# Optimization experiments

Hardware: AMD Instinct MI355X
Metric: run time of the kernel (lower is better)

Reference implementation:

```python
import jax, jax.numpy as jnp
import numpy as np

H = 2048        # hidden_size
I = 1408        # moe_intermediate_size
E = 8           # n_routed_experts
TOP_K = 2       # num_experts_per_tok
N_SHARED = 2
IS = N_SHARED * I  # shared expert intermediate


def setup_inputs() -> dict:
    key = jax.random.key(0)
    ks = jax.random.split(key, 8)
    s_h = 1.0 / np.sqrt(H)
    s_i = 1.0 / np.sqrt(I)
    s_is = 1.0 / np.sqrt(IS)
    return {
        "hidden_states": jax.random.normal(ks[0], (1, 2048, H), jnp.float32),
        "gate_w": jax.random.normal(ks[1], (E, H), jnp.float32) * s_h,
        "w_gate": jax.random.normal(ks[2], (E, H, I), jnp.float32) * s_h,
        "w_up": jax.random.normal(ks[3], (E, H, I), jnp.float32) * s_h,
        "w_down": jax.random.normal(ks[4], (E, I, H), jnp.float32) * s_i,
        "sw_gate": jax.random.normal(ks[5], (H, IS), jnp.float32) * s_h,
        "sw_up": jax.random.normal(ks[6], (H, IS), jnp.float32) * s_h,
        "sw_down": jax.random.normal(ks[7], (IS, H), jnp.float32) * s_is,
    }


def reference(hidden_states, gate_w, w_gate, w_up, w_down, sw_gate, sw_up, sw_down):
    B, S, _ = hidden_states.shape
    x = hidden_states.reshape(-1, H)          # [N, H]
    N = x.shape[0]

    # --- gate: softmax over expert logits, then top-k (DeepSeek greedy gate) ---
    logits = x @ gate_w.T                      # [N, E]
    scores = jax.nn.softmax(logits, axis=-1)
    topk_w, topk_i = jax.lax.top_k(scores, TOP_K)   # [N, K]

    # --- routed experts: dense compute per expert, masked combine ---
    g = jnp.einsum('nh,ehi->eni', x, w_gate)   # [E, N, I]
    u = jnp.einsum('nh,ehi->eni', x, w_up)
    h = jax.nn.silu(g) * u
    eo = jnp.einsum('eni,eih->enh', h, w_down)  # [E, N, H]

    # combine weights: scatter top-k softmax scores into [N, E]
    combine = jnp.zeros((N, E), x.dtype).at[jnp.arange(N)[:, None], topk_i].add(topk_w)
    y = jnp.einsum('ne,enh->nh', combine, eo)  # weighted scatter-reduce combine

    # --- shared experts (always-on SwiGLU MLP) ---
    sh = jax.nn.silu(x @ sw_gate) * (x @ sw_up)
    y = y + sh @ sw_down

    return y.reshape(B, S, H)
```

## Files before the change

### kernel.cpp

```cpp
#include <hip/hip_runtime.h>
#include <hip/hip_bf16.h>

#define H    2048
#define NI   1408
#define NE   8
#define NTOK 2048
#define NIS  2816

typedef __bf16 bf16x8 __attribute__((ext_vector_type(8)));
typedef float  f32x4  __attribute__((ext_vector_type(4)));

#define ASYNC16(gp, lp) __builtin_amdgcn_global_load_lds( \
    (const __attribute__((address_space(1))) void*)(gp),  \
    (__attribute__((address_space(3))) void*)(lp), 16, 0, 0)

__global__ __launch_bounds__(256)
void cvt_kernel(const float* __restrict__ in, __bf16* __restrict__ out)
{
    size_t i = ((size_t)blockIdx.x * 256 + threadIdx.x) * 8;
    float4 v0 = *(const float4*)(in + i);
    float4 v1 = *(const float4*)(in + i + 4);
    union { __bf16 b[8]; uint4 u; } p;
    p.b[0] = (__bf16)v0.x; p.b[1] = (__bf16)v0.y;
    p.b[2] = (__bf16)v0.z; p.b[3] = (__bf16)v0.w;
    p.b[4] = (__bf16)v1.x; p.b[5] = (__bf16)v1.y;
    p.b[6] = (__bf16)v1.z; p.b[7] = (__bf16)v1.w;
    *(uint4*)(out + i) = p.u;
}

__global__ __launch_bounds__(256)
void cvt_t_kernel(const float* __restrict__ in, __bf16* __restrict__ out,
                  int K, int N)
{
    const size_t zoff = (size_t)blockIdx.z * K * N;
    in  += zoff;
    out += zoff;
    const int n0 = blockIdx.x * 64;
    const int k0 = blockIdx.y * 64;
    __shared__ __bf16 tile[64][72];
    const int t = threadIdx.x;
    const int tr  = t >> 4;
    const int tc4 = (t & 15) * 4;
#pragma unroll
    for (int i = 0; i < 4; ++i) {
        int k = i * 16 + tr;
        float4 v = *(const float4*)(in + (size_t)(k0 + k) * N + n0 + tc4);
        tile[k][tc4 + 0] = (__bf16)v.x;
        tile[k][tc4 + 1] = (__bf16)v.y;
        tile[k][tc4 + 2] = (__bf16)v.z;
        tile[k][tc4 + 3] = (__bf16)v.w;
    }
    __syncthreads();
    const int n = t >> 2, q = t & 3;
#pragma unroll
    for (int hh = 0; hh < 2; ++hh) {
        int qq = q + hh * 4;
        union { __bf16 b[8]; uint4 u; } pk;
#pragma unroll
        for (int j = 0; j < 8; ++j) pk.b[j] = tile[qq * 8 + j][n];
        *(uint4*)(out + (size_t)(n0 + n) * K + k0 + qq * 8) = pk.u;
    }
}

__global__ __launch_bounds__(256)
void gate_kernel(const float* __restrict__ x, const float* __restrict__ gw,
                 float* __restrict__ topw, int* __restrict__ pairs,
                 int* __restrict__ cnt)
{
    int tok  = blockIdx.x * 4 + (threadIdx.x >> 6);
    int lane = threadIdx.x & 63;
    float acc[NE];
#pragma unroll
    for (int e = 0; e < NE; ++e) acc[e] = 0.f;
    const float* xr = x + (size_t)tok * H;
    for (int h = lane; h < H; h += 64) {
        float xv = xr[h];
#pragma unroll
        for (int e = 0; e < NE; ++e) acc[e] += xv * gw[e * H + h];
    }
#pragma unroll
    for (int e = 0; e < NE; ++e) {
        float v = acc[e];
        for (int off = 32; off; off >>= 1) v += __shfl_xor(v, off);
        acc[e] = v;
    }
    if (lane == 0) {
        float mx = acc[0];
#pragma unroll
        for (int e = 1; e < NE; ++e) mx = fmaxf(mx, acc[e]);
        float p[NE]; float s = 0.f;
#pragma unroll
        for (int e = 0; e < NE; ++e) { p[e] = __expf(acc[e] - mx); s += p[e]; }
        float inv = 1.f / s;
        int e1 = 0;
#pragma unroll
        for (int e = 1; e < NE; ++e) if (acc[e] > acc[e1]) e1 = e;
        int e2 = -1;
#pragma unroll
        for (int e = 0; e < NE; ++e) {
            if (e == e1) continue;
            if (e2 < 0 || acc[e] > acc[e2]) e2 = e;
        }
        topw[tok * 2 + 0] = p[e1] * inv;
        topw[tok * 2 + 1] = p[e2] * inv;
        int pos1 = atomicAdd(&cnt[e1], 1);
        pairs[e1 * NTOK + pos1] = tok * 2 + 0;
        int pos2 = atomicAdd(&cnt[e2], 1);
        pairs[e2 * NTOK + pos2] = tok * 2 + 1;
    }
}

__global__ __launch_bounds__(256, 2)
void gu_kernel(const __bf16* __restrict__ xb,
               const __bf16* __restrict__ wgT, const __bf16* __restrict__ wuT,
               const __bf16* __restrict__ swgT, const __bf16* __restrict__ swuT,
               __bf16* __restrict__ h_sh, __bf16* __restrict__ h_rt,
               const int* __restrict__ pairs, const int* __restrict__ cnt)
{
    const int t = threadIdx.x, lane = t & 63;
    const int wid = t >> 6, wm = wid >> 1, wn = wid & 1;
    const int e = blockIdx.z;
    const bool routed = (e < NE);
    const int m0 = blockIdx.y * 128, n0 = blockIdx.x * 128;

    int count = NTOK;
    const __bf16 *Bg, *Bu;
    __bf16* outp;
    int ldO;
    if (routed) {
        if (n0 >= NI) return;
        count = cnt[e];
        if (m0 >= count) return;
        Bg = wgT + (size_t)e * NI * H;
        Bu = wuT + (size_t)e * NI * H;
        outp = h_rt; ldO = NI;
    } else {
        Bg = swgT; Bu = swuT; outp = h_sh; ldO = NIS;
    }

    __shared__ __align__(16) __bf16 At[128 * 32], Btg[128 * 32], Btu[128 * 32];
    __shared__ int tile_pid[128];
    if (t < 128) {
        int j = m0 + t;
        tile_pid[t] = routed ? ((j < count) ? pairs[e * NTOK + j] : -1) : j;
    }
    __syncthreads();

    const int r = t >> 2, c = t & 3;
    size_t ar0, ar1;
    if (routed) {
        int p0 = tile_pid[r];      if (p0 < 0) p0 = 0;
        int p1 = tile_pid[r + 64]; if (p1 < 0) p1 = 0;
        ar0 = (size_t)(p0 >> 1); ar1 = (size_t)(p1 >> 1);
    } else {
        ar0 = (size_t)(m0 + r); ar1 = (size_t)(m0 + r + 64);
    }
    const __bf16* a0 = xb + ar0 * H + c * 8;
    const __bf16* a1 = xb + ar1 * H + c * 8;
    const __bf16* g0 = Bg + (size_t)(n0 + r) * H + c * 8;
    const __bf16* g1 = Bg + (size_t)(n0 + r + 64) * H + c * 8;
    const __bf16* u0 = Bu + (size_t)(n0 + r) * H + c * 8;
    const __bf16* u1 = Bu + (size_t)(n0 + r + 64) * H + c * 8;
    __bf16* lA0 = At  + t * 8;  __bf16* lA1 = At  + (256 + t) * 8;
    __bf16* lG0 = Btg + t * 8;  __bf16* lG1 = Btg + (256 + t) * 8;
    __bf16* lU0 = Btu + t * 8;  __bf16* lU1 = Btu + (256 + t) * 8;

    f32x4 accg[4][4] = {};
    f32x4 accu[4][4] = {};

    for (int k0 = 0; k0 < H; k0 += 32) {
        __syncthreads();
        ASYNC16(a0 + k0, lA0); ASYNC16(a1 + k0, lA1);
        ASYNC16(g0 + k0, lG0); ASYNC16(g1 + k0, lG1);
        ASYNC16(u0 + k0, lU0); ASYNC16(u1 + k0, lU1);
        __syncthreads();
        bf16x8 a[4];
#pragma unroll
        for (int mi = 0; mi < 4; ++mi)
            a[mi] = *(const bf16x8*)(At + (wm * 64 + mi * 16 + (lane & 15)) * 32 + (lane >> 4) * 8);
#pragma unroll
        for (int ni = 0; ni < 4; ++ni) {
            bf16x8 bg = *(const bf16x8*)(Btg + (wn * 64 + ni * 16 + (lane & 15)) * 32 + (lane >> 4) * 8);
            bf16x8 bu = *(const bf16x8*)(Btu + (wn * 64 + ni * 16 + (lane & 15)) * 32 + (lane >> 4) * 8);
#pragma unroll
            for (int mi = 0; mi < 4; ++mi) {
                accg[mi][ni] = __builtin_amdgcn_mfma_f32_16x16x32_bf16(a[mi], bg, accg[mi][ni], 0, 0, 0);
                accu[mi][ni] = __builtin_amdgcn_mfma_f32_16x16x32_bf16(a[mi], bu, accu[mi][ni], 0, 0, 0);
            }
        }
    }

#pragma unroll
    for (int mi = 0; mi < 4; ++mi) {
#pragma unroll
        for (int rr = 0; rr < 4; ++rr) {
            int row = wm * 64 + mi * 16 + (lane >> 4) * 4 + rr;
            int pid = tile_pid[row];
            if (routed && pid < 0) continue;
            size_t orow = routed ? (size_t)pid : (size_t)(m0 + row);
#pragma unroll
            for (int ni = 0; ni < 4; ++ni) {
                int col = n0 + wn * 64 + ni * 16 + (lane & 15);
                float g = accg[mi][ni][rr];
                float u = accu[mi][ni][rr];
                float hv = g / (1.f + __expf(-g)) * u;
                outp[orow * (size_t)ldO + col] = (__bf16)hv;
            }
        }
    }
}

__global__ __launch_bounds__(256, 2)
void down_kernel(const __bf16* __restrict__ h_sh, const __bf16* __restrict__ h_rt,
                 const __bf16* __restrict__ swdT, const __bf16* __restrict__ wdT,
                 float* __restrict__ out,
                 const int* __restrict__ pairs, const int* __restrict__ cnt,
                 const float* __restrict__ topw)
{
    const int t = threadIdx.x, lane = t & 63;
    const int wid = t >> 6, wm = wid >> 1, wn = wid & 1;
    const int e = blockIdx.z;
    const bool routed = (e < NE);
    const int m0 = blockIdx.y * 128, n0 = blockIdx.x * 128;

    int count = NTOK, K, lda, koff = 0;
    const __bf16 *A, *B;
    if (routed) {
        count = cnt[e];
        if (m0 >= count) return;
        A = h_rt; lda = NI; K = NI;
        B = wdT + (size_t)e * H * NI;
    } else {
        A = h_sh; lda = NIS; K = NI;
        koff = (e == NE) ? 0 : NI;
        B = swdT;
    }

    __shared__ __align__(16) __bf16 At[128 * 32], Bt[128 * 32];
    __shared__ int tile_pid[128];
    if (t < 128) {
        int j = m0 + t;
        tile_pid[t] = routed ? ((j < count) ? pairs[e * NTOK + j] : -1) : j;
    }
    __syncthreads();

    const int r = t >> 2, c = t & 3;
    size_t ar0, ar1;
    if (routed) {
        int p0 = tile_pid[r];      if (p0 < 0) p0 = 0;
        int p1 = tile_pid[r + 64]; if (p1 < 0) p1 = 0;
        ar0 = (size_t)p0; ar1 = (size_t)p1;
    } else {
        ar0 = (size_t)(m0 + r); ar1 = (size_t)(m0 + r + 64);
    }
    const __bf16* a0 = A + ar0 * lda + koff + c * 8;
    const __bf16* a1 = A + ar1 * lda + koff + c * 8;
    const __bf16* b0 = B + (size_t)(n0 + r) * lda + koff + c * 8;
    const __bf16* b1 = B + (size_t)(n0 + r + 64) * lda + koff + c * 8;
    __bf16* lA0 = At + t * 8;  __bf16* lA1 = At + (256 + t) * 8;
    __bf16* lB0 = Bt + t * 8;  __bf16* lB1 = Bt + (256 + t) * 8;

    f32x4 acc[4][4] = {};

    for (int k0 = 0; k0 < K; k0 += 32) {
        __syncthreads();
        ASYNC16(a0 + k0, lA0); ASYNC16(a1 + k0, lA1);
        ASYNC16(b0 + k0, lB0); ASYNC16(b1 + k0, lB1);
        __syncthreads();
        bf16x8 a[4];
#pragma unroll
        for (int mi = 0; mi < 4; ++mi)
            a[mi] = *(const bf16x8*)(At + (wm * 64 + mi * 16 + (lane & 15)) * 32 + (lane >> 4) * 8);
#pragma unroll
        for (int ni = 0; ni < 4; ++ni) {
            bf16x8 b = *(const bf16x8*)(Bt + (wn * 64 + ni * 16 + (lane & 15)) * 32 + (lane >> 4) * 8);
#pragma unroll
            for (int mi = 0; mi < 4; ++mi)
                acc[mi][ni] = __builtin_amdgcn_mfma_f32_16x16x32_bf16(a[mi], b, acc[mi][ni], 0, 0, 0);
        }
    }

#pragma unroll
    for (int mi = 0; mi < 4; ++mi) {
#pragma unroll
        for (int rr = 0; rr < 4; ++rr) {
            int row = wm * 64 + mi * 16 + (lane >> 4) * 4 + rr;
            int pid = tile_pid[row];
            if (routed && pid < 0) continue;
            size_t tok; float w;
            if (routed) { tok = (size_t)(pid >> 1); w = topw[pid]; }
            else        { tok = (size_t)(m0 + row); w = 1.f; }
#pragma unroll
            for (int ni = 0; ni < 4; ++ni) {
                int col = n0 + wn * 64 + ni * 16 + (lane & 15);
                atomicAdd(out + tok * H + col, w * acc[mi][ni][rr]);
            }
        }
    }
}

extern "C" void kernel_launch(void* const* d_in, const int* in_sizes, int n_in,
                              void* d_out, int out_size, void* d_ws, size_t ws_size,
                              hipStream_t stream)
{
    const float* x       = (const float*)d_in[0];
    const float* gate_w  = (const float*)d_in[1];
    const float* w_gate  = (const float*)d_in[2];
    const float* w_up    = (const float*)d_in[3];
    const float* w_down  = (const float*)d_in[4];
    const float* sw_gate = (const float*)d_in[5];
    const float* sw_up   = (const float*)d_in[6];
    const float* sw_down = (const float*)d_in[7];

    char*   ws    = (char*)d_ws;
    float*  topw  = (float*)ws;
    int*    cnt   = (int*)(ws + 16384);
    int*    pairs = (int*)(ws + 16512);
    __bf16* xb    = (__bf16*)(ws + 131072);
    __bf16* h_sh  = (__bf16*)(ws + 8519680);
    __bf16* h_rt  = (__bf16*)(ws + 20054016);
    __bf16* swgT  = (__bf16*)(ws + 31588352);
    __bf16* swuT  = (__bf16*)(ws + 43122688);
    __bf16* swdT  = (__bf16*)(ws + 54657024);
    __bf16* wgT   = (__bf16*)(ws + 66191360);
    __bf16* wuT   = (__bf16*)(ws + 112328704);
    __bf16* wdT   = wgT;

    hipMemsetAsync(cnt, 0, NE * sizeof(int), stream);
    hipMemsetAsync(d_out, 0, (size_t)NTOK * H * sizeof(float), stream);

    cvt_kernel<<<NTOK * H / 2048, 256, 0, stream>>>(x, xb);
    cvt_t_kernel<<<dim3(NIS / 64, H / 64, 1), 256, 0, stream>>>(sw_gate, swgT, H, NIS);
    cvt_t_kernel<<<dim3(NIS / 64, H / 64, 1), 256, 0, stream>>>(sw_up,   swuT, H, NIS);
    cvt_t_kernel<<<dim3(H / 64, NIS / 64, 1), 256, 0, stream>>>(sw_down, swdT, NIS, H);
    cvt_t_kernel<<<dim3(NI / 64, H / 64, NE), 256, 0, stream>>>(w_gate,  wgT,  H, NI);
    cvt_t_kernel<<<dim3(NI / 64, H / 64, NE), 256, 0, stream>>>(w_up,    wuT,  H, NI);

    gate_kernel<<<NTOK / 4, 256, 0, stream>>>(x, gate_w, topw, pairs, cnt);

    gu_kernel<<<dim3(NIS / 128, NTOK / 128, NE + 1), 256, 0, stream>>>(
        xb, wgT, wuT, swgT, swuT, h_sh, h_rt, pairs, cnt);

    cvt_t_kernel<<<dim3(H / 64, NI / 64, NE), 256, 0, stream>>>(w_down, wdT, NI, H);

    down_kernel<<<dim3(H / 128, NTOK / 128, NE + 2), 256, 0, stream>>>(
        h_sh, h_rt, swdT, wdT, (float*)d_out, pairs, cnt, topw);
}
```

Measured before the change: 687.6 us.

## Rewrite gate/up GEMM with 256x256 tiles, interleaved weights and double-buffered LDS pipeline

The gate and up weights are interleaved in 128-row blocks during conversion, so one 256-wide B tile covers both gate and up columns. The gu kernel moves to 512 threads with 256x256 tiles, a double-buffered swizzled LDS pipeline using async global-to-LDS loads, explicit waitcnt and barriers, and raised priority around MFMA bursts. Up-projection accumulators are passed to the gate warps through LDS for the SiLU epilogue. This targets better data reuse and overlap of loads with MFMA, at the cost of 128KB of LDS per block, lower occupancy, and more padding waste for small routed expert counts.

Result: slower. 723.7 us (+5.2%).

```diff
diff --git a/kernel.cpp b/kernel.cpp
--- a/kernel.cpp
+++ b/kernel.cpp
@@ -13,6 +13,8 @@
 #define ASYNC16(gp, lp) __builtin_amdgcn_global_load_lds( \
     (const __attribute__((address_space(1))) void*)(gp),  \
     (__attribute__((address_space(3))) void*)(lp), 16, 0, 0)
+
+#define MFMA16 __builtin_amdgcn_mfma_f32_16x16x32_bf16
 
 __global__ __launch_bounds__(256)
 void cvt_kernel(const float* __restrict__ in, __bf16* __restrict__ out)
@@ -30,11 +32,10 @@
 
 __global__ __launch_bounds__(256)
 void cvt_t_kernel(const float* __restrict__ in, __bf16* __restrict__ out,
-                  int K, int N)
-{
-    const size_t zoff = (size_t)blockIdx.z * K * N;
-    in  += zoff;
-    out += zoff;
+                  int K, int N, int pmode)
+{
+    in  += (size_t)blockIdx.z * K * N;
+    out += (size_t)blockIdx.z * (pmode < 0 ? (size_t)K * N : 2 * (size_t)K * N);
     const int n0 = blockIdx.x * 64;
     const int k0 = blockIdx.y * 64;
     __shared__ __bf16 tile[64][72];
@@ -58,7 +59,10 @@
         union { __bf16 b[8]; uint4 u; } pk;
 #pragma unroll
         for (int j = 0; j < 8; ++j) pk.b[j] = tile[qq * 8 + j][n];
-        *(uint4*)(out + (size_t)(n0 + n) * K + k0 + qq * 8) = pk.u;
+        int gn = n0 + n;
+        size_t orow = (pmode < 0) ? (size_t)gn
+                    : ((size_t)((gn >> 7) * 2 + pmode) * 128 + (gn & 127));
+        *(uint4*)(out + orow * K + k0 + qq * 8) = pk.u;
     }
 }
 
@@ -110,104 +114,177 @@
     }
 }
 
-__global__ __launch_bounds__(256, 2)
+#define NT (H / 64)
+
+__global__ __launch_bounds__(512, 2)
 void gu_kernel(const __bf16* __restrict__ xb,
-               const __bf16* __restrict__ wgT, const __bf16* __restrict__ wuT,
-               const __bf16* __restrict__ swgT, const __bf16* __restrict__ swuT,
+               const __bf16* __restrict__ wguT, const __bf16* __restrict__ swguT,
                __bf16* __restrict__ h_sh, __bf16* __restrict__ h_rt,
                const int* __restrict__ pairs, const int* __restrict__ cnt)
 {
     const int t = threadIdx.x, lane = t & 63;
-    const int wid = t >> 6, wm = wid >> 1, wn = wid & 1;
+    const int wid = t >> 6;
+    const int wm = wid & 1;
+    const int wn = wid >> 1;
     const int e = blockIdx.z;
     const bool routed = (e < NE);
-    const int m0 = blockIdx.y * 128, n0 = blockIdx.x * 128;
+    const int sb = blockIdx.x;
+    const int m0 = blockIdx.y * 256;
 
     int count = NTOK;
-    const __bf16 *Bg, *Bu;
+    const __bf16* Bp;
     __bf16* outp;
     int ldO;
     if (routed) {
-        if (n0 >= NI) return;
+        if (sb >= NI / 128) return;
         count = cnt[e];
         if (m0 >= count) return;
-        Bg = wgT + (size_t)e * NI * H;
-        Bu = wuT + (size_t)e * NI * H;
+        Bp = wguT + (size_t)e * (2 * NI * H) + (size_t)sb * 256 * H;
         outp = h_rt; ldO = NI;
     } else {
-        Bg = swgT; Bu = swuT; outp = h_sh; ldO = NIS;
-    }
-
-    __shared__ __align__(16) __bf16 At[128 * 32], Btg[128 * 32], Btu[128 * 32];
-    __shared__ int tile_pid[128];
-    if (t < 128) {
+        Bp = swguT + (size_t)sb * 256 * H;
+        outp = h_sh; ldO = NIS;
+    }
+
+    __shared__ __align__(16) __bf16 sm[65536];
+    __shared__ int tile_pid[256];
+#define AH(buf, kk) (sm + ((buf) * 2 + (kk)) * 8192)
+#define BH(buf, kk) (sm + 32768 + ((buf) * 2 + (kk)) * 8192)
+
+    if (t < 256) {
         int j = m0 + t;
         tile_pid[t] = routed ? ((j < count) ? pairs[e * NTOK + j] : -1) : j;
     }
     __syncthreads();
 
-    const int r = t >> 2, c = t & 3;
+    const int sr = t >> 2;
+    const int cg = (t & 3) ^ ((t >> 3) & 3);
     size_t ar0, ar1;
     if (routed) {
-        int p0 = tile_pid[r];      if (p0 < 0) p0 = 0;
-        int p1 = tile_pid[r + 64]; if (p1 < 0) p1 = 0;
+        int p0 = tile_pid[sr];        if (p0 < 0) p0 = 0;
+        int p1 = tile_pid[128 + sr];  if (p1 < 0) p1 = 0;
         ar0 = (size_t)(p0 >> 1); ar1 = (size_t)(p1 >> 1);
     } else {
-        ar0 = (size_t)(m0 + r); ar1 = (size_t)(m0 + r + 64);
-    }
-    const __bf16* a0 = xb + ar0 * H + c * 8;
-    const __bf16* a1 = xb + ar1 * H + c * 8;
-    const __bf16* g0 = Bg + (size_t)(n0 + r) * H + c * 8;
-    const __bf16* g1 = Bg + (size_t)(n0 + r + 64) * H + c * 8;
-    const __bf16* u0 = Bu + (size_t)(n0 + r) * H + c * 8;
-    const __bf16* u1 = Bu + (size_t)(n0 + r + 64) * H + c * 8;
-    __bf16* lA0 = At  + t * 8;  __bf16* lA1 = At  + (256 + t) * 8;
-    __bf16* lG0 = Btg + t * 8;  __bf16* lG1 = Btg + (256 + t) * 8;
-    __bf16* lU0 = Btu + t * 8;  __bf16* lU1 = Btu + (256 + t) * 8;
-
-    f32x4 accg[4][4] = {};
-    f32x4 accu[4][4] = {};
-
-    for (int k0 = 0; k0 < H; k0 += 32) {
-        __syncthreads();
-        ASYNC16(a0 + k0, lA0); ASYNC16(a1 + k0, lA1);
-        ASYNC16(g0 + k0, lG0); ASYNC16(g1 + k0, lG1);
-        ASYNC16(u0 + k0, lU0); ASYNC16(u1 + k0, lU1);
-        __syncthreads();
-        bf16x8 a[4];
-#pragma unroll
-        for (int mi = 0; mi < 4; ++mi)
-            a[mi] = *(const bf16x8*)(At + (wm * 64 + mi * 16 + (lane & 15)) * 32 + (lane >> 4) * 8);
-#pragma unroll
-        for (int ni = 0; ni < 4; ++ni) {
-            bf16x8 bg = *(const bf16x8*)(Btg + (wn * 64 + ni * 16 + (lane & 15)) * 32 + (lane >> 4) * 8);
-            bf16x8 bu = *(const bf16x8*)(Btu + (wn * 64 + ni * 16 + (lane & 15)) * 32 + (lane >> 4) * 8);
-#pragma unroll
-            for (int mi = 0; mi < 4; ++mi) {
-                accg[mi][ni] = __builtin_amdgcn_mfma_f32_16x16x32_bf16(a[mi], bg, accg[mi][ni], 0, 0, 0);
-                accu[mi][ni] = __builtin_amdgcn_mfma_f32_16x16x32_bf16(a[mi], bu, accu[mi][ni], 0, 0, 0);
+        ar0 = (size_t)(m0 + sr); ar1 = (size_t)(m0 + 128 + sr);
+    }
+    const __bf16* gA0 = xb + ar0 * H + cg * 8;
+    const __bf16* gA1 = xb + ar1 * H + cg * 8;
+    const __bf16* gB0 = Bp + (size_t)sr * H + cg * 8;
+    const __bf16* gB1 = Bp + (size_t)(128 + sr) * H + cg * 8;
+
+#define STAGE_A(T, kk, buf) do {                              \
+        ASYNC16(gA0 + (T) * 64 + (kk) * 32, AH(buf, kk) + t * 8);        \
+        ASYNC16(gA1 + (T) * 64 + (kk) * 32, AH(buf, kk) + 4096 + t * 8); \
+    } while (0)
+#define STAGE_B(T, kk, buf) do {                              \
+        ASYNC16(gB0 + (T) * 64 + (kk) * 32, BH(buf, kk) + t * 8);        \
+        ASYNC16(gB1 + (T) * 64 + (kk) * 32, BH(buf, kk) + 4096 + t * 8); \
+    } while (0)
+
+    const int fr  = lane & 15;
+    const int cr8 = (((lane >> 4) ^ ((fr >> 1) & 3)) << 3);
+    const int aoff = (wm * 128 + fr) * 32 + cr8;
+    const int boff = (wn * 64  + fr) * 32 + cr8;
+
+    f32x4 acc[8][4] = {};
+    bf16x8 a[8], b[2];
+
+    STAGE_A(0, 0, 0); STAGE_B(0, 0, 0);
+    STAGE_A(0, 1, 0); STAGE_B(0, 1, 0);
+    STAGE_A(1, 0, 1); STAGE_B(1, 0, 1);
+    asm volatile("s_waitcnt vmcnt(4)" ::: "memory");
+    __builtin_amdgcn_s_barrier();
+
+#define PHASE_MFMA(NHB)                                       \
+    __builtin_amdgcn_s_barrier();                             \
+    asm volatile("s_waitcnt lgkmcnt(0)" ::: "memory");        \
+    __builtin_amdgcn_sched_barrier(0);                        \
+    __builtin_amdgcn_s_setprio(1);                            \
+    _Pragma("unroll")                                         \
+    for (int mi = 0; mi < 8; ++mi) {                          \
+        acc[mi][(NHB) + 0] = MFMA16(a[mi], b[0], acc[mi][(NHB) + 0], 0, 0, 0); \
+        acc[mi][(NHB) + 1] = MFMA16(a[mi], b[1], acc[mi][(NHB) + 1], 0, 0, 0); \
+    }                                                         \
+    __builtin_amdgcn_s_setprio(0);                            \
+    __builtin_amdgcn_s_barrier();
+
+#define TILE(TT, BUF) do {                                                   \
+                \
+    _Pragma("unroll")                                                        \
+    for (int mi = 0; mi < 8; ++mi)                                           \
+        a[mi] = *(const bf16x8*)(AH(BUF, 0) + aoff + mi * 512);              \
+    b[0] = *(const bf16x8*)(BH(BUF, 0) + boff);                              \
+    b[1] = *(const bf16x8*)(BH(BUF, 0) + boff + 512);                        \
+    if ((TT) + 1 < NT) { STAGE_A((TT) + 1, 1, (BUF) ^ 1);                    \
+                         STAGE_B((TT) + 1, 1, (BUF) ^ 1); }                  \
+    PHASE_MFMA(0)                                                            \
+                                                    \
+    b[0] = *(const bf16x8*)(BH(BUF, 0) + boff + 1024);                       \
+    b[1] = *(const bf16x8*)(BH(BUF, 0) + boff + 1536);                       \
+    PHASE_MFMA(2)                                                            \
+                  \
+    _Pragma("unroll")                                                        \
+    for (int mi = 0; mi < 8; ++mi)                                           \
+        a[mi] = *(const bf16x8*)(AH(BUF, 1) + aoff + mi * 512);              \
+    b[0] = *(const bf16x8*)(BH(BUF, 1) + boff);                              \
+    b[1] = *(const bf16x8*)(BH(BUF, 1) + boff + 512);                        \
+    if ((TT) + 2 < NT) STAGE_A((TT) + 2, 0, BUF);                            \
+    PHASE_MFMA(0)                                                            \
+           \
+    b[0] = *(const bf16x8*)(BH(BUF, 1) + boff + 1024);                       \
+    b[1] = *(const bf16x8*)(BH(BUF, 1) + boff + 1536);                       \
+    if ((TT) + 2 < NT) STAGE_B((TT) + 2, 0, BUF);                            \
+    if ((TT) + 2 < NT) asm volatile("s_waitcnt vmcnt(4)" ::: "memory");      \
+    else               asm volatile("s_waitcnt vmcnt(0)" ::: "memory");      \
+    PHASE_MFMA(2)                                                            \
+} while (0)
+
+#pragma unroll 1
+    for (int tt = 0; tt < NT; tt += 2) {
+        TILE(tt, 0);
+        TILE(tt + 1, 1);
+    }
+
+    float* uls = (float*)sm;
+    if (wn >= 2) {
+#pragma unroll
+        for (int mi = 0; mi < 8; ++mi)
+#pragma unroll
+            for (int rr = 0; rr < 4; ++rr) {
+                int row = wm * 128 + mi * 16 + (lane >> 4) * 4 + rr;
+#pragma unroll
+                for (int ni = 0; ni < 4; ++ni) {
+                    int col = (wn - 2) * 64 + ni * 16 + (lane & 15);
+                    uls[row * 128 + col] = acc[mi][ni][rr];
+                }
             }
-        }
-    }
-
-#pragma unroll
-    for (int mi = 0; mi < 4; ++mi) {
-#pragma unroll
-        for (int rr = 0; rr < 4; ++rr) {
-            int row = wm * 64 + mi * 16 + (lane >> 4) * 4 + rr;
-            int pid = tile_pid[row];
-            if (routed && pid < 0) continue;
-            size_t orow = routed ? (size_t)pid : (size_t)(m0 + row);
-#pragma unroll
-            for (int ni = 0; ni < 4; ++ni) {
-                int col = n0 + wn * 64 + ni * 16 + (lane & 15);
-                float g = accg[mi][ni][rr];
-                float u = accu[mi][ni][rr];
-                float hv = g / (1.f + __expf(-g)) * u;
-                outp[orow * (size_t)ldO + col] = (__bf16)hv;
+    }
+    __syncthreads();
+    if (wn < 2) {
+#pragma unroll
+        for (int mi = 0; mi < 8; ++mi)
+#pragma unroll
+            for (int rr = 0; rr < 4; ++rr) {
+                int row = wm * 128 + mi * 16 + (lane >> 4) * 4 + rr;
+                int pid = tile_pid[row];
+                if (routed && pid < 0) continue;
+                size_t orow = routed ? (size_t)pid : (size_t)(m0 + row);
+#pragma unroll
+                for (int ni = 0; ni < 4; ++ni) {
+                    int lc = wn * 64 + ni * 16 + (lane & 15);
+                    float g = acc[mi][ni][rr];
+                    float u = uls[row * 128 + lc];
+                    float hv = g / (1.f + __expf(-g)) * u;
+                    outp[orow * (size_t)ldO + sb * 128 + lc] = (__bf16)hv;
+                }
             }
-        }
-    }
+    }
+#undef AH
+#undef BH
+#undef STAGE_A
+#undef STAGE_B
+#undef PHASE_MFMA
+#undef TILE
 }
 
 __global__ __launch_bounds__(256, 2)
@@ -319,29 +396,27 @@
     __bf16* xb    = (__bf16*)(ws + 131072);
     __bf16* h_sh  = (__bf16*)(ws + 8519680);
     __bf16* h_rt  = (__bf16*)(ws + 20054016);
-    __bf16* swgT  = (__bf16*)(ws + 31588352);
-    __bf16* swuT  = (__bf16*)(ws + 43122688);
+    __bf16* swguT = (__bf16*)(ws + 31588352);
     __bf16* swdT  = (__bf16*)(ws + 54657024);
-    __bf16* wgT   = (__bf16*)(ws + 66191360);
-    __bf16* wuT   = (__bf16*)(ws + 112328704);
-    __bf16* wdT   = wgT;
+    __bf16* wguT  = (__bf16*)(ws + 66191360);
+    __bf16* wdT   = wguT;
 
     hipMemsetAsync(cnt, 0, NE * sizeof(int), stream);
     hipMemsetAsync(d_out, 0, (size_t)NTOK * H * sizeof(float), stream);
 
     cvt_kernel<<<NTOK * H / 2048, 256, 0, stream>>>(x, xb);
-    cvt_t_kernel<<<dim3(NIS / 64, H / 64, 1), 256, 0, stream>>>(sw_gate, swgT, H, NIS);
-    cvt_t_kernel<<<dim3(NIS / 64, H / 64, 1), 256, 0, stream>>>(sw_up,   swuT, H, NIS);
-    cvt_t_kernel<<<dim3(H / 64, NIS / 64, 1), 256, 0, stream>>>(sw_down, swdT, NIS, H);
-    cvt_t_kernel<<<dim3(NI / 64, H / 64, NE), 256, 0, stream>>>(w_gate,  wgT,  H, NI);
-    cvt_t_kernel<<<dim3(NI / 64, H / 64, NE), 256, 0, stream>>>(w_up,    wuT,  H, NI);
+    cvt_t_kernel<<<dim3(NIS / 64, H / 64, 1), 256, 0, stream>>>(sw_gate, swguT, H, NIS, 0);
+    cvt_t_kernel<<<dim3(NIS / 64, H / 64, 1), 256, 0, stream>>>(sw_up,   swguT, H, NIS, 1);
+    cvt_t_kernel<<<dim3(H / 64, NIS / 64, 1), 256, 0, stream>>>(sw_down, swdT, NIS, H, -1);
+    cvt_t_kernel<<<dim3(NI / 64, H / 64, NE), 256, 0, stream>>>(w_gate,  wguT, H, NI, 0);
+    cvt_t_kernel<<<dim3(NI / 64, H / 64, NE), 256, 0, stream>>>(w_up,    wguT, H, NI, 1);
 
     gate_kernel<<<NTOK / 4, 256, 0, stream>>>(x, gate_w, topw, pairs, cnt);
 
-    gu_kernel<<<dim3(NIS / 128, NTOK / 128, NE + 1), 256, 0, stream>>>(
-        xb, wgT, wuT, swgT, swuT, h_sh, h_rt, pairs, cnt);
-
-    cvt_t_kernel<<<dim3(H / 64, NI / 64, NE), 256, 0, stream>>>(w_down, wdT, NI, H);
+    gu_kernel<<<dim3(NIS / 128, NTOK / 256, NE + 1), 512, 0, stream>>>(
+        xb, wguT, swguT, h_sh, h_rt, pairs, cnt);
+
+    cvt_t_kernel<<<dim3(H / 64, NI / 64, NE), 256, 0, stream>>>(w_down, wdT, NI, H, -1);
 
     down_kernel<<<dim3(H / 128, NTOK / 128, NE + 2), 256, 0, stream>>>(
         h_sh, h_rt, swdT, wdT, (float*)d_out, pairs, cnt, topw);
```

## Double-buffer LDS with XOR swizzle and split shared down-proj to plain stores

Applied to the files above, without the earlier changes.

The gate/up and down GEMM loops now prefetch the next K tile into a second LDS buffer while computing on the current one, which removes one barrier per iteration. The global-to-LDS column mapping and the fragment reads use an XOR swizzle to reduce LDS bank conflicts. The shared-expert down projection moves to its own kernel over the full K=2816 that writes output directly, replacing the output memset and two atomic K-halves. The routed down kernel then atomically adds on top of that output, which depends on stream ordering. LDS use doubles, which may lower occupancy.

Result: no change. 698.8 us (+1.6%).

```diff
diff --git a/kernel.cpp b/kernel.cpp
--- a/kernel.cpp
+++ b/kernel.cpp
@@ -13,6 +13,8 @@
 #define ASYNC16(gp, lp) __builtin_amdgcn_global_load_lds( \
     (const __attribute__((address_space(1))) void*)(gp),  \
     (__attribute__((address_space(3))) void*)(lp), 16, 0, 0)
+
+#define MFMA16 __builtin_amdgcn_mfma_f32_16x16x32_bf16
 
 __global__ __launch_bounds__(256)
 void cvt_kernel(const float* __restrict__ in, __bf16* __restrict__ out)
@@ -138,7 +140,7 @@
         Bg = swgT; Bu = swuT; outp = h_sh; ldO = NIS;
     }
 
-    __shared__ __align__(16) __bf16 At[128 * 32], Btg[128 * 32], Btu[128 * 32];
+    __shared__ __align__(16) __bf16 At[2 * 4096], Btg[2 * 4096], Btu[2 * 4096];
     __shared__ int tile_pid[128];
     if (t < 128) {
         int j = m0 + t;
@@ -146,7 +148,8 @@
     }
     __syncthreads();
 
-    const int r = t >> 2, c = t & 3;
+    const int r = t >> 2;
+    const int cg = (t & 3) ^ ((t >> 3) & 3);
     size_t ar0, ar1;
     if (routed) {
         int p0 = tile_pid[r];      if (p0 < 0) p0 = 0;
@@ -155,40 +158,52 @@
     } else {
         ar0 = (size_t)(m0 + r); ar1 = (size_t)(m0 + r + 64);
     }
-    const __bf16* a0 = xb + ar0 * H + c * 8;
-    const __bf16* a1 = xb + ar1 * H + c * 8;
-    const __bf16* g0 = Bg + (size_t)(n0 + r) * H + c * 8;
-    const __bf16* g1 = Bg + (size_t)(n0 + r + 64) * H + c * 8;
-    const __bf16* u0 = Bu + (size_t)(n0 + r) * H + c * 8;
-    const __bf16* u1 = Bu + (size_t)(n0 + r + 64) * H + c * 8;
-    __bf16* lA0 = At  + t * 8;  __bf16* lA1 = At  + (256 + t) * 8;
-    __bf16* lG0 = Btg + t * 8;  __bf16* lG1 = Btg + (256 + t) * 8;
-    __bf16* lU0 = Btu + t * 8;  __bf16* lU1 = Btu + (256 + t) * 8;
+    const __bf16* a0 = xb + ar0 * H + cg * 8;
+    const __bf16* a1 = xb + ar1 * H + cg * 8;
+    const __bf16* g0 = Bg + (size_t)(n0 + r) * H + cg * 8;
+    const __bf16* g1 = Bg + (size_t)(n0 + r + 64) * H + cg * 8;
+    const __bf16* u0 = Bu + (size_t)(n0 + r) * H + cg * 8;
+    const __bf16* u1 = Bu + (size_t)(n0 + r + 64) * H + cg * 8;
+
+#define STAGE_GU(k, bo) do {                              \
+        ASYNC16(a0 + (k), At  + (bo) + t * 8);            \
+        ASYNC16(a1 + (k), At  + (bo) + 2048 + t * 8);     \
+        ASYNC16(g0 + (k), Btg + (bo) + t * 8);            \
+        ASYNC16(g1 + (k), Btg + (bo) + 2048 + t * 8);     \
+        ASYNC16(u0 + (k), Btu + (bo) + t * 8);            \
+        ASYNC16(u1 + (k), Btu + (bo) + 2048 + t * 8);     \
+    } while (0)
+
+    const int fr  = lane & 15;
+    const int cr8 = (((lane >> 4) ^ ((fr >> 1) & 3)) << 3);
 
     f32x4 accg[4][4] = {};
     f32x4 accu[4][4] = {};
 
+    STAGE_GU(0, 0);
+    __syncthreads();
+
+    int bo = 0;
     for (int k0 = 0; k0 < H; k0 += 32) {
+        if (k0 + 32 < H) STAGE_GU(k0 + 32, bo ^ 4096);
+        bf16x8 a[4];
+#pragma unroll
+        for (int mi = 0; mi < 4; ++mi)
+            a[mi] = *(const bf16x8*)(At + bo + (wm * 64 + mi * 16 + fr) * 32 + cr8);
+#pragma unroll
+        for (int ni = 0; ni < 4; ++ni) {
+            bf16x8 bg = *(const bf16x8*)(Btg + bo + (wn * 64 + ni * 16 + fr) * 32 + cr8);
+            bf16x8 bu = *(const bf16x8*)(Btu + bo + (wn * 64 + ni * 16 + fr) * 32 + cr8);
+#pragma unroll
+            for (int mi = 0; mi < 4; ++mi) {
+                accg[mi][ni] = MFMA16(a[mi], bg, accg[mi][ni], 0, 0, 0);
+                accu[mi][ni] = MFMA16(a[mi], bu, accu[mi][ni], 0, 0, 0);
+            }
+        }
         __syncthreads();
-        ASYNC16(a0 + k0, lA0); ASYNC16(a1 + k0, lA1);
-        ASYNC16(g0 + k0, lG0); ASYNC16(g1 + k0, lG1);
-        ASYNC16(u0 + k0, lU0); ASYNC16(u1 + k0, lU1);
-        __syncthreads();
-        bf16x8 a[4];
-#pragma unroll
-        for (int mi = 0; mi < 4; ++mi)
-            a[mi] = *(const bf16x8*)(At + (wm * 64 + mi * 16 + (lane & 15)) * 32 + (lane >> 4) * 8);
-#pragma unroll
-        for (int ni = 0; ni < 4; ++ni) {
-            bf16x8 bg = *(const bf16x8*)(Btg + (wn * 64 + ni * 16 + (lane & 15)) * 32 + (lane >> 4) * 8);
-            bf16x8 bu = *(const bf16x8*)(Btu + (wn * 64 + ni * 16 + (lane & 15)) * 32 + (lane >> 4) * 8);
-#pragma unroll
-            for (int mi = 0; mi < 4; ++mi) {
-                accg[mi][ni] = __builtin_amdgcn_mfma_f32_16x16x32_bf16(a[mi], bg, accg[mi][ni], 0, 0, 0);
-                accu[mi][ni] = __builtin_amdgcn_mfma_f32_16x16x32_bf16(a[mi], bu, accu[mi][ni], 0, 0, 0);
-            }
-        }
-    }
+        bo ^= 4096;
+    }
+#undef STAGE_GU
 
 #pragma unroll
     for (int mi = 0; mi < 4; ++mi) {
@@ -211,74 +226,127 @@
 }
 
 __global__ __launch_bounds__(256, 2)
-void down_kernel(const __bf16* __restrict__ h_sh, const __bf16* __restrict__ h_rt,
-                 const __bf16* __restrict__ swdT, const __bf16* __restrict__ wdT,
-                 float* __restrict__ out,
-                 const int* __restrict__ pairs, const int* __restrict__ cnt,
-                 const float* __restrict__ topw)
+void down_sh_kernel(const __bf16* __restrict__ h_sh, const __bf16* __restrict__ swdT,
+                    float* __restrict__ out)
+{
+    const int t = threadIdx.x, lane = t & 63;
+    const int wid = t >> 6, wm = wid >> 1, wn = wid & 1;
+    const int m0 = blockIdx.y * 128, n0 = blockIdx.x * 128;
+
+    __shared__ __align__(16) __bf16 At[2 * 4096], Bt[2 * 4096];
+
+    const int r = t >> 2;
+    const int cg = (t & 3) ^ ((t >> 3) & 3);
+    const __bf16* a0 = h_sh + (size_t)(m0 + r) * NIS + cg * 8;
+    const __bf16* a1 = h_sh + (size_t)(m0 + r + 64) * NIS + cg * 8;
+    const __bf16* b0 = swdT + (size_t)(n0 + r) * NIS + cg * 8;
+    const __bf16* b1 = swdT + (size_t)(n0 + r + 64) * NIS + cg * 8;
+
+#define STAGE_D(k, bo) do {                               \
+        ASYNC16(a0 + (k), At + (bo) + t * 8);             \
+        ASYNC16(a1 + (k), At + (bo) + 2048 + t * 8);      \
+        ASYNC16(b0 + (k), Bt + (bo) + t * 8);             \
+        ASYNC16(b1 + (k), Bt + (bo) + 2048 + t * 8);      \
+    } while (0)
+
+    const int fr  = lane & 15;
+    const int cr8 = (((lane >> 4) ^ ((fr >> 1) & 3)) << 3);
+
+    f32x4 acc[4][4] = {};
+
+    STAGE_D(0, 0);
+    __syncthreads();
+
+    int bo = 0;
+    for (int k0 = 0; k0 < NIS; k0 += 32) {
+        if (k0 + 32 < NIS) STAGE_D(k0 + 32, bo ^ 4096);
+        bf16x8 a[4];
+#pragma unroll
+        for (int mi = 0; mi < 4; ++mi)
+            a[mi] = *(const bf16x8*)(At + bo + (wm * 64 + mi * 16 + fr) * 32 + cr8);
+#pragma unroll
+        for (int ni = 0; ni < 4; ++ni) {
+            bf16x8 b = *(const bf16x8*)(Bt + bo + (wn * 64 + ni * 16 + fr) * 32 + cr8);
+#pragma unroll
+            for (int mi = 0; mi < 4; ++mi)
+                acc[mi][ni] = MFMA16(a[mi], b, acc[mi][ni], 0, 0, 0);
+        }
+        __syncthreads();
+        bo ^= 4096;
+    }
+
+#pragma unroll
+    for (int mi = 0; mi < 4; ++mi) {
+#pragma unroll
+        for (int rr = 0; rr < 4; ++rr) {
+            int row = wm * 64 + mi * 16 + (lane >> 4) * 4 + rr;
+#pragma unroll
+            for (int ni = 0; ni < 4; ++ni) {
+                int col = n0 + wn * 64 + ni * 16 + (lane & 15);
+                out[(size_t)(m0 + row) * H + col] = acc[mi][ni][rr];
+            }
+        }
+    }
+}
+
+__global__ __launch_bounds__(256, 2)
+void down_rt_kernel(const __bf16* __restrict__ h_rt, const __bf16* __restrict__ wdT,
+                    float* __restrict__ out,
+                    const int* __restrict__ pairs, const int* __restrict__ cnt,
+                    const float* __restrict__ topw)
 {
     const int t = threadIdx.x, lane = t & 63;
     const int wid = t >> 6, wm = wid >> 1, wn = wid & 1;
     const int e = blockIdx.z;
-    const bool routed = (e < NE);
     const int m0 = blockIdx.y * 128, n0 = blockIdx.x * 128;
 
-    int count = NTOK, K, lda, koff = 0;
-    const __bf16 *A, *B;
-    if (routed) {
-        count = cnt[e];
-        if (m0 >= count) return;
-        A = h_rt; lda = NI; K = NI;
-        B = wdT + (size_t)e * H * NI;
-    } else {
-        A = h_sh; lda = NIS; K = NI;
-        koff = (e == NE) ? 0 : NI;
-        B = swdT;
-    }
-
-    __shared__ __align__(16) __bf16 At[128 * 32], Bt[128 * 32];
+    const int count = cnt[e];
+    if (m0 >= count) return;
+    const __bf16* B = wdT + (size_t)e * H * NI;
+
+    __shared__ __align__(16) __bf16 At[2 * 4096], Bt[2 * 4096];
     __shared__ int tile_pid[128];
     if (t < 128) {
         int j = m0 + t;
-        tile_pid[t] = routed ? ((j < count) ? pairs[e * NTOK + j] : -1) : j;
-    }
-    __syncthreads();
-
-    const int r = t >> 2, c = t & 3;
-    size_t ar0, ar1;
-    if (routed) {
-        int p0 = tile_pid[r];      if (p0 < 0) p0 = 0;
-        int p1 = tile_pid[r + 64]; if (p1 < 0) p1 = 0;
-        ar0 = (size_t)p0; ar1 = (size_t)p1;
-    } else {
-        ar0 = (size_t)(m0 + r); ar1 = (size_t)(m0 + r + 64);
-    }
-    const __bf16* a0 = A + ar0 * lda + koff + c * 8;
-    const __bf16* a1 = A + ar1 * lda + koff + c * 8;
-    const __bf16* b0 = B + (size_t)(n0 + r) * lda + koff + c * 8;
-    const __bf16* b1 = B + (size_t)(n0 + r + 64) * lda + koff + c * 8;
-    __bf16* lA0 = At + t * 8;  __bf16* lA1 = At + (256 + t) * 8;
-    __bf16* lB0 = Bt + t * 8;  __bf16* lB1 = Bt + (256 + t) * 8;
+        tile_pid[t] = (j < count) ? pairs[e * NTOK + j] : -1;
+    }
+    __syncthreads();
+
+    const int r = t >> 2;
+    const int cg = (t & 3) ^ ((t >> 3) & 3);
+    int p0 = tile_pid[r];      if (p0 < 0) p0 = 0;
+    int p1 = tile_pid[r + 64]; if (p1 < 0) p1 = 0;
+    const __bf16* a0 = h_rt + (size_t)p0 * NI + cg * 8;
+    const __bf16* a1 = h_rt + (size_t)p1 * NI + cg * 8;
+    const __bf16* b0 = B + (size_t)(n0 + r) * NI + cg * 8;
+    const __bf16* b1 = B + (size_t)(n0 + r + 64) * NI + cg * 8;
+
+    const int fr  = lane & 15;
+    const int cr8 = (((lane >> 4) ^ ((fr >> 1) & 3)) << 3);
 
     f32x4 acc[4][4] = {};
 
-    for (int k0 = 0; k0 < K; k0 += 32) {
+    STAGE_D(0, 0);
+    __syncthreads();
+
+    int bo = 0;
+    for (int k0 = 0; k0 < NI; k0 += 32) {
+        if (k0 + 32 < NI) STAGE_D(k0 + 32, bo ^ 4096);
+        bf16x8 a[4];
+#pragma unroll
+        for (int mi = 0; mi < 4; ++mi)
+            a[mi] = *(const bf16x8*)(At + bo + (wm * 64 + mi * 16 + fr) * 32 + cr8);
+#pragma unroll
+        for (int ni = 0; ni < 4; ++ni) {
+            bf16x8 b = *(const bf16x8*)(Bt + bo + (wn * 64 + ni * 16 + fr) * 32 + cr8);
+#pragma unroll
+            for (int mi = 0; mi < 4; ++mi)
+                acc[mi][ni] = MFMA16(a[mi], b, acc[mi][ni], 0, 0, 0);
+        }
         __syncthreads();
-        ASYNC16(a0 + k0, lA0); ASYNC16(a1 + k0, lA1);
-        ASYNC16(b0 + k0, lB0); ASYNC16(b1 + k0, lB1);
-        __syncthreads();
-        bf16x8 a[4];
-#pragma unroll
-        for (int mi = 0; mi < 4; ++mi)
-            a[mi] = *(const bf16x8*)(At + (wm * 64 + mi * 16 + (lane & 15)) * 32 + (lane >> 4) * 8);
-#pragma unroll
-        for (int ni = 0; ni < 4; ++ni) {
-            bf16x8 b = *(const bf16x8*)(Bt + (wn * 64 + ni * 16 + (lane & 15)) * 32 + (lane >> 4) * 8);
-#pragma unroll
-            for (int mi = 0; mi < 4; ++mi)
-                acc[mi][ni] = __builtin_amdgcn_mfma_f32_16x16x32_bf16(a[mi], b, acc[mi][ni], 0, 0, 0);
-        }
-    }
+        bo ^= 4096;
+    }
+#undef STAGE_D
 
 #pragma unroll
     for (int mi = 0; mi < 4; ++mi) {
@@ -286,10 +354,9 @@
         for (int rr = 0; rr < 4; ++rr) {
             int row = wm * 64 + mi * 16 + (lane >> 4) * 4 + rr;
             int pid = tile_pid[row];
-            if (routed && pid < 0) continue;
-            size_t tok; float w;
-            if (routed) { tok = (size_t)(pid >> 1); w = topw[pid]; }
-            else        { tok = (size_t)(m0 + row); w = 1.f; }
+            if (pid < 0) continue;
+            size_t tok = (size_t)(pid >> 1);
+            float w = topw[pid];
 #pragma unroll
             for (int ni = 0; ni < 4; ++ni) {
                 int col = n0 + wn * 64 + ni * 16 + (lane & 15);
@@ -327,7 +394,6 @@
     __bf16* wdT   = wgT;
 
     hipMemsetAsync(cnt, 0, NE * sizeof(int), stream);
-    hipMemsetAsync(d_out, 0, (size_t)NTOK * H * sizeof(float), stream);
 
     cvt_kernel<<<NTOK * H / 2048, 256, 0, stream>>>(x, xb);
     cvt_t_kernel<<<dim3(NIS / 64, H / 64, 1), 256, 0, stream>>>(sw_gate, swgT, H, NIS);
@@ -341,8 +407,11 @@
     gu_kernel<<<dim3(NIS / 128, NTOK / 128, NE + 1), 256, 0, stream>>>(
         xb, wgT, wuT, swgT, swuT, h_sh, h_rt, pairs, cnt);
 
+    down_sh_kernel<<<dim3(H / 128, NTOK / 128, 1), 256, 0, stream>>>(
+        h_sh, swdT, (float*)d_out);
+
     cvt_t_kernel<<<dim3(H / 64, NI / 64, NE), 256, 0, stream>>>(w_down, wdT, NI, H);
 
-    down_kernel<<<dim3(H / 128, NTOK / 128, NE + 2), 256, 0, stream>>>(
-        h_sh, h_rt, swdT, wdT, (float*)d_out, pairs, cnt, topw);
-}
+    down_rt_kernel<<<dim3(H / 128, NTOK / 128, NE), 256, 0, stream>>>(
+        h_rt, wdT, (float*)d_out, pairs, cnt, topw);
+}
```
